# Kernel tuning notes

Hardware: AMD Instinct MI355X
Metric: run time of the kernel (lower is better)

Reference implementation:

```python
import jax, jax.numpy as jnp
import numpy as np

NUM_HEADS = 16
KERNEL_SIZE = 13  # odd, neighborhood size nh = 6


def setup_inputs() -> dict:
    key = jax.random.key(0)
    ks = jax.random.split(key, 6)
    B, L, C = 4, 4096, 512
    return {
        "x": jax.random.normal(ks[0], (B, L, C), dtype=jnp.float32),
        "qkv_w": jax.random.normal(ks[1], (3 * C, C), dtype=jnp.float32) * (C ** -0.5),
        "qkv_b": jax.random.normal(ks[2], (3 * C,), dtype=jnp.float32) * 0.02,
        "rpb": jax.random.normal(ks[3], (NUM_HEADS, 2 * KERNEL_SIZE - 1), dtype=jnp.float32) * 0.02,
        "proj_w": jax.random.normal(ks[4], (C, C), dtype=jnp.float32) * (C ** -0.5),
        "proj_b": jax.random.normal(ks[5], (C,), dtype=jnp.float32) * 0.02,
    }


def reference(x, qkv_w, qkv_b, rpb, proj_w, proj_b):
    B, L, C = x.shape
    H, K = NUM_HEADS, KERNEL_SIZE
    Dh = C // H
    scale = Dh ** -0.5
    nh = K // 2

    # qkv projection (torch Linear: x @ W.T + b)
    qkv = (x @ qkv_w.T + qkv_b).reshape(B, L, 3, H, Dh)
    qkv = jnp.transpose(qkv, (2, 0, 3, 1, 4))  # (3, B, H, L, Dh)
    q, k, v = qkv[0] * scale, qkv[1], qkv[2]

    # neighborhood indices: window of K keys, shifted (not clipped) at borders
    pos = jnp.arange(L)
    start = jnp.clip(pos - nh, 0, L - K)            # (L,)
    idx = start[:, None] + jnp.arange(K)[None, :]   # (L, K) key positions
    # relative-position-bias index: (key_pos - query_pos) + (K-1), in [0, 2K-2]
    bias_idx = idx - pos[:, None] + (K - 1)         # (L, K)

    k_g = k[:, :, idx, :]                           # (B, H, L, K, Dh)
    attn = jnp.einsum('bhld,bhlkd->bhlk', q, k_g)   # (B, H, L, K)
    attn = attn + rpb[:, bias_idx][None]            # add (H, L, K) bias
    attn = jax.nn.softmax(attn, axis=-1)

    v_g = v[:, :, idx, :]                           # (B, H, L, K, Dh)
    out = jnp.einsum('bhlk,bhlkd->bhld', attn, v_g)  # (B, H, L, Dh)
    out = jnp.transpose(out, (0, 2, 1, 3)).reshape(B, L, C)
    return out @ proj_w.T + proj_b
```

## Files before the change

### kernel.cpp

```cpp
#include <hip/hip_runtime.h>
#include <hip/hip_bf16.h>

#define BATCH   4
#define LSEQ    4096
#define CCH     512
#define HNUM    16
#define DH      32
#define KSZ     13
#define NHALF   6
#define M_TOT   16384
#define N_QKV   1536
#define KDIM    512
#define BK      64

typedef __attribute__((ext_vector_type(8))) short  short8;
typedef __attribute__((ext_vector_type(4))) short  short4_t;
typedef __attribute__((ext_vector_type(4))) float  float4_t;

__device__ __forceinline__ unsigned short f32_to_bf16(float f) {
    union { float f; unsigned int u; } un; un.f = f;
    unsigned int u = un.u;
    u += 0x7FFFu + ((u >> 16) & 1u);
    return (unsigned short)(u >> 16);
}
__device__ __forceinline__ float bf16_to_f32(unsigned short h) {
    union { unsigned int u; float f; } un; un.u = ((unsigned int)h) << 16;
    return un.f;
}

__device__ __forceinline__ void gload_lds16(const unsigned short* g, unsigned short* l) {
    __builtin_amdgcn_global_load_lds(
        (const __attribute__((address_space(1))) unsigned int*)g,
        (__attribute__((address_space(3))) unsigned int*)l,
        16, 0, 0);
}

__global__ void cvt_f32_bf16_v4(const float4_t* __restrict__ in,
                                short4_t* __restrict__ out, int n4) {
    int i = blockIdx.x * blockDim.x + threadIdx.x;
    int stride = gridDim.x * blockDim.x;
    for (; i < n4; i += stride) {
        float4_t v = in[i];
        short4_t h;
        h.x = (short)f32_to_bf16(v.x);
        h.y = (short)f32_to_bf16(v.y);
        h.z = (short)f32_to_bf16(v.z);
        h.w = (short)f32_to_bf16(v.w);
        out[i] = h;
    }
}

__global__ __launch_bounds__(256) void gemm_qkv(
    const unsigned short* __restrict__ Xb,
    const unsigned short* __restrict__ W,
    const float* __restrict__ bias,
    unsigned short* __restrict__ qkvout)
{
    __shared__ __align__(16) unsigned short As[128 * BK];
    __shared__ __align__(16) unsigned short Bs[128 * BK];
    const int tid  = threadIdx.x;
    const int wv   = tid >> 6, ln = tid & 63;
    const int m0   = blockIdx.x * 128;
    const int n0   = blockIdx.y * 128;
    const int wm   = (wv >> 1) * 64;
    const int wn   = (wv & 1) * 64;
    const int lr   = ln & 15;
    const int lg   = ln >> 4;
    const int rgrp = ln >> 3;
    const int csw  = ((ln & 7) ^ rgrp) * 8;

    float4_t acc[4][4];
    #pragma unroll
    for (int m = 0; m < 4; ++m)
        #pragma unroll
        for (int n = 0; n < 4; ++n)
            acc[m][n] = (float4_t){0.f, 0.f, 0.f, 0.f};

    for (int k0 = 0; k0 < KDIM; k0 += BK) {
        #pragma unroll
        for (int it = 0; it < 4; ++it) {
            int ch  = it * 4 + wv;
            int row = ch * 8 + rgrp;
            gload_lds16(Xb + (size_t)(m0 + row) * KDIM + k0 + csw,
                        &As[ch * 8 * BK]);
            gload_lds16(W  + (size_t)(n0 + row) * KDIM + k0 + csw,
                        &Bs[ch * 8 * BK]);
        }
        __syncthreads();
        short8 af[2][4], bfr[2][4];
        #pragma unroll
        for (int kk = 0; kk < 2; ++kk) {
            #pragma unroll
            for (int m = 0; m < 4; ++m) {
                int row = wm + m * 16 + lr;
                int c   = (kk * 4 + lg) ^ (row & 7);
                af[kk][m] = *reinterpret_cast<const short8*>(&As[row * BK + c * 8]);
            }
            #pragma unroll
            for (int n = 0; n < 4; ++n) {
                int row = wn + n * 16 + lr;
                int c   = (kk * 4 + lg) ^ (row & 7);
                bfr[kk][n] = *reinterpret_cast<const short8*>(&Bs[row * BK + c * 8]);
            }
        }
        #pragma unroll
        for (int kk = 0; kk < 2; ++kk)
            #pragma unroll
            for (int m = 0; m < 4; ++m)
                #pragma unroll
                for (int n = 0; n < 4; ++n)
                    acc[m][n] = __builtin_amdgcn_mfma_f32_16x16x32_bf16(
                        af[kk][m], bfr[kk][n], acc[m][n], 0, 0, 0);
        __syncthreads();
    }

    const float qscale = 0.17677669529663687f;
    #pragma unroll
    for (int m = 0; m < 4; ++m) {
        #pragma unroll
        for (int n = 0; n < 4; ++n) {
            int gn    = n0 + wn + n * 16 + lr;
            int which = gn >> 9;
            int hh    = (gn >> 5) & 15;
            int dd    = gn & 31;
            float bsv = bias[gn];
            #pragma unroll
            for (int r = 0; r < 4; ++r) {
                int gm = m0 + wm + m * 16 + lg * 4 + r;
                float v = acc[m][n][r] + bsv;
                if (which == 0) v *= qscale;
                int b_ = gm >> 12, l = gm & 4095;
                size_t off = (((size_t)which * BATCH + b_) * HNUM + hh) *
                                 ((size_t)LSEQ * DH) + (size_t)l * DH + dd;
                qkvout[off] = f32_to_bf16(v);
            }
        }
    }
}

__global__ __launch_bounds__(256) void natten_fwd(
    const unsigned short* __restrict__ qkv,
    const float* __restrict__ rpb,
    unsigned short* __restrict__ ctx)
{
    __shared__ unsigned short ks[268 * DH];
    __shared__ unsigned short vs[268 * DH];
    __shared__ float rpb_s[2 * KSZ - 1];

    const int t    = threadIdx.x;
    const int lblk = blockIdx.x & 15;
    const int bh   = blockIdx.x >> 4;
    const int hh   = bh & 15, b_ = bh >> 4;
    const int l0   = lblk * 256;

    const int r0    = max(l0 - NHALF, 0);
    const int rend  = min(l0 + 256 + NHALF, LSEQ);
    const int nrows = rend - r0;

    const size_t plane = (size_t)LSEQ * DH;
    const size_t kbase = (((size_t)1 * BATCH + b_) * HNUM + hh) * plane;
    const size_t vbase = (((size_t)2 * BATCH + b_) * HNUM + hh) * plane;

    for (int slot = t; slot < nrows * 4; slot += 256) {
        int row = slot >> 2, cq = slot & 3;
        *reinterpret_cast<short8*>(&ks[row * DH + cq * 8]) =
            *reinterpret_cast<const short8*>(&qkv[kbase + (size_t)(r0 + row) * DH + cq * 8]);
        *reinterpret_cast<short8*>(&vs[row * DH + cq * 8]) =
            *reinterpret_cast<const short8*>(&qkv[vbase + (size_t)(r0 + row) * DH + cq * 8]);
    }
    if (t < 2 * KSZ - 1) rpb_s[t] = rpb[hh * (2 * KSZ - 1) + t];
    __syncthreads();

    const int l = l0 + t;
    float q[DH];
    const size_t qoff = (((size_t)0 * BATCH + b_) * HNUM + hh) * plane + (size_t)l * DH;
    #pragma unroll
    for (int cq = 0; cq < 4; ++cq) {
        short8 qv = *reinterpret_cast<const short8*>(&qkv[qoff + cq * 8]);
        #pragma unroll
        for (int e = 0; e < 8; ++e) q[cq * 8 + e] = bf16_to_f32((unsigned short)qv[e]);
    }

    const int start = min(max(l - NHALF, 0), LSEQ - KSZ);
    float logit[KSZ];
    #pragma unroll
    for (int j = 0; j < KSZ; ++j) {
        int kr = start + j - r0;
        float s = 0.f;
        #pragma unroll
        for (int cq = 0; cq < 4; ++cq) {
            short8 kv = *reinterpret_cast<const short8*>(&ks[kr * DH + cq * 8]);
            #pragma unroll
            for (int e = 0; e < 8; ++e)
                s += q[cq * 8 + e] * bf16_to_f32((unsigned short)kv[e]);
        }
        logit[j] = s + rpb_s[start + j - l + (KSZ - 1)];
    }
    float mx = logit[0];
    #pragma unroll
    for (int j = 1; j < KSZ; ++j) mx = fmaxf(mx, logit[j]);
    float p[KSZ], sum = 0.f;
    #pragma unroll
    for (int j = 0; j < KSZ; ++j) { p[j] = __expf(logit[j] - mx); sum += p[j]; }
    const float inv = 1.f / sum;

    float o[DH];
    #pragma unroll
    for (int d = 0; d < DH; ++d) o[d] = 0.f;
    #pragma unroll
    for (int j = 0; j < KSZ; ++j) {
        int kr = start + j - r0;
        float pj = p[j] * inv;
        #pragma unroll
        for (int cq = 0; cq < 4; ++cq) {
            short8 vv = *reinterpret_cast<const short8*>(&vs[kr * DH + cq * 8]);
            #pragma unroll
            for (int e = 0; e < 8; ++e)
                o[cq * 8 + e] += pj * bf16_to_f32((unsigned short)vv[e]);
        }
    }
    const size_t obase = ((size_t)(b_ * LSEQ + l)) * CCH + hh * DH;
    #pragma unroll
    for (int cq = 0; cq < 4; ++cq) {
        short8 ov;
        #pragma unroll
        for (int e = 0; e < 8; ++e) ov[e] = (short)f32_to_bf16(o[cq * 8 + e]);
        *reinterpret_cast<short8*>(&ctx[obase + cq * 8]) = ov;
    }
}

__global__ __launch_bounds__(256) void gemm_proj(
    const unsigned short* __restrict__ Xb,
    const unsigned short* __restrict__ W,
    const float* __restrict__ bias,
    float* __restrict__ out)
{
    __shared__ __align__(16) unsigned short As[128 * BK];
    __shared__ __align__(16) unsigned short Bs[128 * BK];
    const int tid  = threadIdx.x;
    const int wv   = tid >> 6, ln = tid & 63;
    const int m0   = blockIdx.x * 128;
    const int n0   = blockIdx.y * 128;
    const int wm   = (wv >> 1) * 64;
    const int wn   = (wv & 1) * 64;
    const int lr   = ln & 15;
    const int lg   = ln >> 4;
    const int rgrp = ln >> 3;
    const int csw  = ((ln & 7) ^ rgrp) * 8;

    float4_t acc[4][4];
    #pragma unroll
    for (int m = 0; m < 4; ++m)
        #pragma unroll
        for (int n = 0; n < 4; ++n)
            acc[m][n] = (float4_t){0.f, 0.f, 0.f, 0.f};

    for (int k0 = 0; k0 < KDIM; k0 += BK) {
        #pragma unroll
        for (int it = 0; it < 4; ++it) {
            int ch  = it * 4 + wv;
            int row = ch * 8 + rgrp;
            gload_lds16(Xb + (size_t)(m0 + row) * KDIM + k0 + csw,
                        &As[ch * 8 * BK]);
            gload_lds16(W  + (size_t)(n0 + row) * KDIM + k0 + csw,
                        &Bs[ch * 8 * BK]);
        }
        __syncthreads();
        short8 af[2][4], bfr[2][4];
        #pragma unroll
        for (int kk = 0; kk < 2; ++kk) {
            #pragma unroll
            for (int m = 0; m < 4; ++m) {
                int row = wm + m * 16 + lr;
                int c   = (kk * 4 + lg) ^ (row & 7);
                af[kk][m] = *reinterpret_cast<const short8*>(&As[row * BK + c * 8]);
            }
            #pragma unroll
            for (int n = 0; n < 4; ++n) {
                int row = wn + n * 16 + lr;
                int c   = (kk * 4 + lg) ^ (row & 7);
                bfr[kk][n] = *reinterpret_cast<const short8*>(&Bs[row * BK + c * 8]);
            }
        }
        #pragma unroll
        for (int kk = 0; kk < 2; ++kk)
            #pragma unroll
            for (int m = 0; m < 4; ++m)
                #pragma unroll
                for (int n = 0; n < 4; ++n)
                    acc[m][n] = __builtin_amdgcn_mfma_f32_16x16x32_bf16(
                        af[kk][m], bfr[kk][n], acc[m][n], 0, 0, 0);
        __syncthreads();
    }

    #pragma unroll
    for (int m = 0; m < 4; ++m) {
        #pragma unroll
        for (int n = 0; n < 4; ++n) {
            int gn = n0 + wn + n * 16 + lr;
            float bsv = bias[gn];
            #pragma unroll
            for (int r = 0; r < 4; ++r) {
                int gm = m0 + wm + m * 16 + lg * 4 + r;
                out[(size_t)gm * CCH + gn] = acc[m][n][r] + bsv;
            }
        }
    }
}

extern "C" void kernel_launch(void* const* d_in, const int* in_sizes, int n_in,
                              void* d_out, int out_size, void* d_ws, size_t ws_size,
                              hipStream_t stream) {
    const float* x      = (const float*)d_in[0];
    const float* qkv_w  = (const float*)d_in[1];
    const float* qkv_b  = (const float*)d_in[2];
    const float* rpb    = (const float*)d_in[3];
    const float* proj_w = (const float*)d_in[4];
    const float* proj_b = (const float*)d_in[5];
    float* out = (float*)d_out;
    char* ws = (char*)d_ws;

    unsigned short* qkv = (unsigned short*)(ws);
    unsigned short* xb  = (unsigned short*)(ws + 50331648);
    unsigned short* ctx = (unsigned short*)(ws + 50331648);
    unsigned short* wq  = (unsigned short*)(ws + 67108864);
    unsigned short* wp  = (unsigned short*)(ws + 68681728);

    cvt_f32_bf16_v4<<<2048, 256, 0, stream>>>((const float4_t*)x, (short4_t*)xb, M_TOT * KDIM / 4);
    cvt_f32_bf16_v4<<<768, 256, 0, stream>>>((const float4_t*)qkv_w, (short4_t*)wq, 786432 / 4);
    cvt_f32_bf16_v4<<<256, 256, 0, stream>>>((const float4_t*)proj_w, (short4_t*)wp, 262144 / 4);

    dim3 g1(M_TOT / 128, N_QKV / 128);
    gemm_qkv<<<g1, 256, 0, stream>>>(xb, wq, qkv_b, qkv);

    natten_fwd<<<BATCH * HNUM * (LSEQ / 256), 256, 0, stream>>>(qkv, rpb, ctx);

    dim3 g2(M_TOT / 128, CCH / 128);
    gemm_proj<<<g2, 256, 0, stream>>>(ctx, wp, proj_b, out);
}
```

Measured before the change: 88.17 us.

## Double-buffer QKV GEMM with 256x256 tiles, XCD swizzle, and split natten LDS layout

The QKV GEMM is restructured into 256x256 tiles with 8 waves and double-buffered LDS (128KB dynamic shared memory). The next K-tile load now overlaps MFMA work through vmcnt waits, setprio and sched barriers, and a block-index swizzle groups tiles across XCDs for L2 reuse. The natten kernel's K/V shared-memory layout changes to a column-quarter-major layout so that per-thread short8 reads avoid bank conflicts. The risks are lower occupancy from the large LDS footprint and correctness of the hand-tuned wait counts and barriers.

Measured after the change: 91.49 us. +3.8%, slower.

```diff
diff --git a/kernel.cpp b/kernel.cpp
--- a/kernel.cpp
+++ b/kernel.cpp
@@ -50,84 +50,117 @@
     }
 }
 
-__global__ __launch_bounds__(256) void gemm_qkv(
+__global__ __launch_bounds__(512, 2) void gemm_qkv(
     const unsigned short* __restrict__ Xb,
     const unsigned short* __restrict__ W,
     const float* __restrict__ bias,
     unsigned short* __restrict__ qkvout)
 {
-    __shared__ __align__(16) unsigned short As[128 * BK];
-    __shared__ __align__(16) unsigned short Bs[128 * BK];
+    extern __shared__ __align__(16) unsigned short lds[];
     const int tid  = threadIdx.x;
     const int wv   = tid >> 6, ln = tid & 63;
-    const int m0   = blockIdx.x * 128;
-    const int n0   = blockIdx.y * 128;
-    const int wm   = (wv >> 1) * 64;
-    const int wn   = (wv & 1) * 64;
+
+    const int wg   = blockIdx.x;
+    const int swz  = (wg & 7) * 48 + (wg >> 3);
+    const int m0   = (swz & 63) * 256;
+    const int n0   = (swz >> 6) * 256;
+
+    const int wm   = (wv >> 2) * 128;
+    const int wn   = (wv & 3) * 64;
     const int lr   = ln & 15;
     const int lg   = ln >> 4;
     const int rgrp = ln >> 3;
     const int csw  = ((ln & 7) ^ rgrp) * 8;
 
-    float4_t acc[4][4];
-    #pragma unroll
-    for (int m = 0; m < 4; ++m)
+    float4_t acc[8][4];
+    #pragma unroll
+    for (int m = 0; m < 8; ++m)
         #pragma unroll
         for (int n = 0; n < 4; ++n)
             acc[m][n] = (float4_t){0.f, 0.f, 0.f, 0.f};
 
-    for (int k0 = 0; k0 < KDIM; k0 += BK) {
-        #pragma unroll
-        for (int it = 0; it < 4; ++it) {
-            int ch  = it * 4 + wv;
-            int row = ch * 8 + rgrp;
-            gload_lds16(Xb + (size_t)(m0 + row) * KDIM + k0 + csw,
-                        &As[ch * 8 * BK]);
-            gload_lds16(W  + (size_t)(n0 + row) * KDIM + k0 + csw,
-                        &Bs[ch * 8 * BK]);
-        }
-        __syncthreads();
-        short8 af[2][4], bfr[2][4];
-        #pragma unroll
-        for (int kk = 0; kk < 2; ++kk) {
-            #pragma unroll
-            for (int m = 0; m < 4; ++m) {
-                int row = wm + m * 16 + lr;
-                int c   = (kk * 4 + lg) ^ (row & 7);
-                af[kk][m] = *reinterpret_cast<const short8*>(&As[row * BK + c * 8]);
-            }
-            #pragma unroll
-            for (int n = 0; n < 4; ++n) {
-                int row = wn + n * 16 + lr;
-                int c   = (kk * 4 + lg) ^ (row & 7);
-                bfr[kk][n] = *reinterpret_cast<const short8*>(&Bs[row * BK + c * 8]);
-            }
-        }
-        #pragma unroll
-        for (int kk = 0; kk < 2; ++kk)
-            #pragma unroll
-            for (int m = 0; m < 4; ++m)
+    #define STAGE(t_, buf_) do {                                              \
+        const int k0_ = (t_) * BK;                                            \
+        _Pragma("unroll")                                                     \
+        for (int c4 = 0; c4 < 4; ++c4) {                                      \
+            int r_ = wv * 32 + c4 * 8;                                        \
+            gload_lds16(Xb + (size_t)(m0 + r_ + rgrp) * KDIM + k0_ + csw,     \
+                        &lds[(buf_) * 16384 + r_ * 64]);                      \
+            gload_lds16(W  + (size_t)(n0 + r_ + rgrp) * KDIM + k0_ + csw,     \
+                        &lds[32768 + (buf_) * 16384 + r_ * 64]);              \
+        }                                                                     \
+    } while (0)
+
+    STAGE(0, 0);
+
+    #pragma unroll 2
+    for (int t = 0; t < 8; ++t) {
+        const int buf = t & 1;
+        if (t < 7) {
+            STAGE(t + 1, buf ^ 1);
+            asm volatile("s_waitcnt vmcnt(8)" ::: "memory");
+        } else {
+            asm volatile("s_waitcnt vmcnt(0)" ::: "memory");
+        }
+        __builtin_amdgcn_s_barrier();
+
+        const unsigned short* Ab = &lds[buf * 16384];
+        const unsigned short* Bb = &lds[32768 + buf * 16384];
+
+        short8 af[2][4], bf[2][2];
+        #pragma unroll
+        for (int qm = 0; qm < 2; ++qm) {
+            #pragma unroll
+            for (int kk = 0; kk < 2; ++kk)
                 #pragma unroll
-                for (int n = 0; n < 4; ++n)
-                    acc[m][n] = __builtin_amdgcn_mfma_f32_16x16x32_bf16(
-                        af[kk][m], bfr[kk][n], acc[m][n], 0, 0, 0);
-        __syncthreads();
-    }
+                for (int m = 0; m < 4; ++m) {
+                    int row = wm + qm * 64 + m * 16 + lr;
+                    int c   = (kk * 4 + lg) ^ (lr & 7);
+                    af[kk][m] = *reinterpret_cast<const short8*>(&Ab[row * 64 + c * 8]);
+                }
+            #pragma unroll
+            for (int qn = 0; qn < 2; ++qn) {
+                #pragma unroll
+                for (int kk = 0; kk < 2; ++kk)
+                    #pragma unroll
+                    for (int n = 0; n < 2; ++n) {
+                        int row = wn + qn * 32 + n * 16 + lr;
+                        int c   = (kk * 4 + lg) ^ (lr & 7);
+                        bf[kk][n] = *reinterpret_cast<const short8*>(&Bb[row * 64 + c * 8]);
+                    }
+                __builtin_amdgcn_s_barrier();
+                __builtin_amdgcn_sched_barrier(0);
+                __builtin_amdgcn_s_setprio(1);
+                #pragma unroll
+                for (int kk = 0; kk < 2; ++kk)
+                    #pragma unroll
+                    for (int m = 0; m < 4; ++m)
+                        #pragma unroll
+                        for (int n = 0; n < 2; ++n)
+                            acc[qm * 4 + m][qn * 2 + n] =
+                                __builtin_amdgcn_mfma_f32_16x16x32_bf16(
+                                    af[kk][m], bf[kk][n],
+                                    acc[qm * 4 + m][qn * 2 + n], 0, 0, 0);
+                __builtin_amdgcn_s_setprio(0);
+            }
+        }
+    }
+    #undef STAGE
 
     const float qscale = 0.17677669529663687f;
     #pragma unroll
-    for (int m = 0; m < 4; ++m) {
-        #pragma unroll
-        for (int n = 0; n < 4; ++n) {
-            int gn    = n0 + wn + n * 16 + lr;
+    for (int mf = 0; mf < 8; ++mf) {
+        #pragma unroll
+        for (int nf = 0; nf < 4; ++nf) {
+            int gn    = n0 + wn + nf * 16 + lr;
             int which = gn >> 9;
             int hh    = (gn >> 5) & 15;
             int dd    = gn & 31;
             float bsv = bias[gn];
             #pragma unroll
             for (int r = 0; r < 4; ++r) {
-                int gm = m0 + wm + m * 16 + lg * 4 + r;
-                float v = acc[m][n][r] + bsv;
+                int gm = m0 + wm + mf * 16 + lg * 4 + r;
+                float v = acc[mf][nf][r] + bsv;
                 if (which == 0) v *= qscale;
                 int b_ = gm >> 12, l = gm & 4095;
                 size_t off = (((size_t)which * BATCH + b_) * HNUM + hh) *
@@ -143,8 +176,8 @@
     const float* __restrict__ rpb,
     unsigned short* __restrict__ ctx)
 {
-    __shared__ unsigned short ks[268 * DH];
-    __shared__ unsigned short vs[268 * DH];
+    __shared__ __align__(16) unsigned short ks[4 * 268 * 8];
+    __shared__ __align__(16) unsigned short vs[4 * 268 * 8];
     __shared__ float rpb_s[2 * KSZ - 1];
 
     const int t    = threadIdx.x;
@@ -161,12 +194,19 @@
     const size_t kbase = (((size_t)1 * BATCH + b_) * HNUM + hh) * plane;
     const size_t vbase = (((size_t)2 * BATCH + b_) * HNUM + hh) * plane;
 
-    for (int slot = t; slot < nrows * 4; slot += 256) {
-        int row = slot >> 2, cq = slot & 3;
-        *reinterpret_cast<short8*>(&ks[row * DH + cq * 8]) =
-            *reinterpret_cast<const short8*>(&qkv[kbase + (size_t)(r0 + row) * DH + cq * 8]);
-        *reinterpret_cast<short8*>(&vs[row * DH + cq * 8]) =
-            *reinterpret_cast<const short8*>(&qkv[vbase + (size_t)(r0 + row) * DH + cq * 8]);
+    {
+        const int cq  = t >> 6;
+        const int rr  = t & 63;
+        #pragma unroll
+        for (int base = 0; base < 320; base += 64) {
+            int row = base + rr;
+            if (row < nrows) {
+                *reinterpret_cast<short8*>(&ks[(cq * 268 + row) * 8]) =
+                    *reinterpret_cast<const short8*>(&qkv[kbase + (size_t)(r0 + row) * DH + cq * 8]);
+                *reinterpret_cast<short8*>(&vs[(cq * 268 + row) * 8]) =
+                    *reinterpret_cast<const short8*>(&qkv[vbase + (size_t)(r0 + row) * DH + cq * 8]);
+            }
+        }
     }
     if (t < 2 * KSZ - 1) rpb_s[t] = rpb[hh * (2 * KSZ - 1) + t];
     __syncthreads();
@@ -189,7 +229,7 @@
         float s = 0.f;
         #pragma unroll
         for (int cq = 0; cq < 4; ++cq) {
-            short8 kv = *reinterpret_cast<const short8*>(&ks[kr * DH + cq * 8]);
+            short8 kv = *reinterpret_cast<const short8*>(&ks[(cq * 268 + kr) * 8]);
             #pragma unroll
             for (int e = 0; e < 8; ++e)
                 s += q[cq * 8 + e] * bf16_to_f32((unsigned short)kv[e]);
@@ -213,7 +253,7 @@
         float pj = p[j] * inv;
         #pragma unroll
         for (int cq = 0; cq < 4; ++cq) {
-            short8 vv = *reinterpret_cast<const short8*>(&vs[kr * DH + cq * 8]);
+            short8 vv = *reinterpret_cast<const short8*>(&vs[(cq * 268 + kr) * 8]);
             #pragma unroll
             for (int e = 0; e < 8; ++e)
                 o[cq * 8 + e] += pj * bf16_to_f32((unsigned short)vv[e]);
@@ -330,8 +370,7 @@
     cvt_f32_bf16_v4<<<768, 256, 0, stream>>>((const float4_t*)qkv_w, (short4_t*)wq, 786432 / 4);
     cvt_f32_bf16_v4<<<256, 256, 0, stream>>>((const float4_t*)proj_w, (short4_t*)wp, 262144 / 4);
 
-    dim3 g1(M_TOT / 128, N_QKV / 128);
-    gemm_qkv<<<g1, 256, 0, stream>>>(xb, wq, qkv_b, qkv);
+    gemm_qkv<<<384, 512, 131072, stream>>>(xb, wq, qkv_b, qkv);
 
     natten_fwd<<<BATCH * HNUM * (LSEQ / 256), 256, 0, stream>>>(qkv, rpb, ctx);
 
```
